# Kernel optimization log

Measured on AMD Instinct MI355X. Metric: run time of the kernel, lower is better.

The kernel has to match this reference:

```python
import jax, jax.numpy as jnp
import numpy as np

B, S, D = 8, 2048, 1024


def setup_inputs() -> dict:
    key = jax.random.key(0)
    ks = jax.random.split(key, 10)
    s = 0.02
    x = jax.random.normal(ks[0], (B, S, D), dtype=jnp.float32)
    # causal boolean mask [B, S, S]
    mask = jnp.broadcast_to(jnp.tril(jnp.ones((S, S), dtype=bool)), (B, S, S))
    Wq = jax.random.normal(ks[1], (D, D), dtype=jnp.float32) * s
    bq = jax.random.normal(ks[2], (D,), dtype=jnp.float32) * s
    Wk = jax.random.normal(ks[3], (D, D), dtype=jnp.float32) * s
    bk = jax.random.normal(ks[4], (D,), dtype=jnp.float32) * s
    Wv = jax.random.normal(ks[5], (D, D), dtype=jnp.float32) * s
    bv = jax.random.normal(ks[6], (D,), dtype=jnp.float32) * s
    Wo = jax.random.normal(ks[7], (D, D), dtype=jnp.float32) * s
    bo = jax.random.normal(ks[8], (D,), dtype=jnp.float32) * s
    return {"x": x, "mask": mask, "Wq": Wq, "bq": bq, "Wk": Wk, "bk": bk,
            "Wv": Wv, "bv": bv, "Wo": Wo, "bo": bo}


def reference(x, mask, Wq, bq, Wk, bk, Wv, bv, Wo, bo):
    # no cache -> cache_len = 0, full x/mask used; dropout=0.0 (identity)
    d_k = x.shape[-1]
    q = jnp.einsum('bsd,ed->bse', x, Wq) + bq
    k = jnp.einsum('bsd,ed->bse', x, Wk) + bk  # computed but unused (original bug)
    v = jnp.einsum('bsd,ed->bse', x, Wv) + bv
    # NOTE: original code uses q @ v^T (not k) - reproduced faithfully
    scores = jnp.einsum('bqd,bkd->bqk', q, v) / jnp.sqrt(jnp.float32(d_k))
    scores = jnp.where(mask, scores, jnp.float32(-jnp.inf))
    attn = jax.nn.softmax(scores, axis=-1)
    ctx = jnp.einsum('bqk,bkd->bqd', attn, v)
    out = jnp.einsum('bsd,ed->bse', ctx, Wo) + bo
    return out
```

## Files before the change

### kernel.cpp

```cpp
#include <hip/hip_runtime.h>

typedef unsigned short u16;
typedef __attribute__((ext_vector_type(8))) unsigned short u16x8;
typedef __bf16 bf16x8 __attribute__((ext_vector_type(8)));
typedef float f32x4 __attribute__((ext_vector_type(4)));

__device__ __forceinline__ u16 f2b(float f) {
    unsigned u = __float_as_uint(f);
    u += 0x7fffu + ((u >> 16) & 1u);
    return (u16)(u >> 16);
}
__device__ __forceinline__ float b2f(u16 h) {
    return __uint_as_float(((unsigned)h) << 16);
}

__device__ __forceinline__ void async_copy16(const void* g, void* l) {
    __builtin_amdgcn_global_load_lds(
        (const __attribute__((address_space(1))) unsigned int*)g,
        (__attribute__((address_space(3))) unsigned int*)l,
        16, 0, 0);
}

__device__ __forceinline__ int swz(int x) { return x ^ (((x >> 9) & 1) << 5); }

__global__ __launch_bounds__(256) void cast_kernel(const float* __restrict__ in,
                                                   u16* __restrict__ out, long n) {
    long i0 = ((long)blockIdx.x * 256 + threadIdx.x) * 8;
    long stride = (long)gridDim.x * 256 * 8;
    for (long i = i0; i < n; i += stride) {
        float4 a = *(const float4*)(in + i);
        float4 b = *(const float4*)(in + i + 4);
        u16x8 o;
        o[0] = f2b(a.x); o[1] = f2b(a.y); o[2] = f2b(a.z); o[3] = f2b(a.w);
        o[4] = f2b(b.x); o[5] = f2b(b.y); o[6] = f2b(b.z); o[7] = f2b(b.w);
        *(u16x8*)(out + i) = o;
    }
}

__global__ __launch_bounds__(256) void transpose_kernel(const u16* __restrict__ in,
                                                        u16* __restrict__ out,
                                                        int rows, int cols) {
    __shared__ u16 tile[32][33];
    long base = (long)blockIdx.z * rows * cols;
    const u16* I = in + base;
    u16* O = out + base;
    int r0 = blockIdx.y * 32, c0 = blockIdx.x * 32;
    int tx = threadIdx.x, ty = threadIdx.y;
    #pragma unroll
    for (int j = ty; j < 32; j += 8)
        tile[j][tx] = I[(long)(r0 + j) * cols + c0 + tx];
    __syncthreads();
    #pragma unroll
    for (int j = ty; j < 32; j += 8)
        O[(long)(c0 + j) * rows + r0 + tx] = tile[tx][j];
}

__global__ __launch_bounds__(256) void softmax_kernel(u16* __restrict__ Sc) {
    const int SS = 2048;
    long row = blockIdx.x;
    int q = (int)(row & (SS - 1));
    int L = q + 1;
    int Klim = ((q >> 8) + 1) << 8;
    u16* p = Sc + row * SS;
    int tid = threadIdx.x;

    float m = -1e30f;
    for (int i = tid; i < L; i += 256) m = fmaxf(m, b2f(p[i]));
    #pragma unroll
    for (int o = 32; o > 0; o >>= 1) m = fmaxf(m, __shfl_xor(m, o));
    __shared__ float redm[4];
    if ((tid & 63) == 0) redm[tid >> 6] = m;
    __syncthreads();
    m = fmaxf(fmaxf(redm[0], redm[1]), fmaxf(redm[2], redm[3]));

    float s = 0.f;
    for (int i = tid; i < L; i += 256) s += __expf(b2f(p[i]) - m);
    #pragma unroll
    for (int o = 32; o > 0; o >>= 1) s += __shfl_xor(s, o);
    __shared__ float reds[4];
    if ((tid & 63) == 0) reds[tid >> 6] = s;
    __syncthreads();
    s = reds[0] + reds[1] + reds[2] + reds[3];
    float inv = 1.f / s;

    for (int i = tid; i < Klim; i += 256) {
        float v = (i < L) ? __expf(b2f(p[i]) - m) * inv : 0.f;
        p[i] = f2b(v);
    }
}

template<typename OUTT, bool BIAS, bool CSKIP, bool KLIM>
__global__ __launch_bounds__(512)
void gemm256(const u16* __restrict__ Aall, const u16* __restrict__ Ball,
             const float* __restrict__ bias, OUTT* __restrict__ Call,
             int M, int N, int K, float scale, long sA, long sB, long sC) {
    const int bz = blockIdx.z;
    const u16* A = Aall + (long)bz * sA;
    const u16* B = Ball + (long)bz * sB;
    OUTT* C = Call + (long)bz * sC;
    const int bm = blockIdx.y, bn = blockIdx.x;
    if (CSKIP && bn > bm) return;
    int Keff = K;
    if (KLIM) { int kl = (bm + 1) * 256; Keff = kl < K ? kl : K; }
    const int NT = Keff >> 6;

    extern __shared__ __align__(16) char lds[];

    const int tid = threadIdx.x;
    const int lane = tid & 63;
    const int w = tid >> 6;
    const int wm = w >> 2, wn = w & 3;
    const int fr = lane & 15, hi = lane >> 4;
    const int axor = ((fr >> 2) & 1) << 5;

    const long rowA0 = (long)bm * 256;
    const long rowB0 = (long)bn * 256;

    auto stage_half = [&](const u16* mat, long gr0, int k0, char* region) {
        #pragma unroll
        for (int rd = 0; rd < 2; ++rd) {
            int pb = rd * 8192 + w * 1024;
            int p = pb + lane * 16;
            int L = swz(p);
            const u16* src = mat + (gr0 + (L >> 7)) * (long)K + k0 + ((L & 127) >> 1);
            async_copy16(src, region + pb);
        }
    };

    f32x4 acc[8][4] = {};
    bf16x8 a[4][2], b0[2][2], b1[2][2];

    char* bufp0 = lds;
    char* bufp1 = lds + 65536;

    stage_half(A, rowA0,       0, bufp0 + 0 * 16384);
    stage_half(B, rowB0,       0, bufp0 + 2 * 16384);
    stage_half(B, rowB0 + 128, 0, bufp0 + 3 * 16384);
    stage_half(A, rowA0 + 128, 0, bufp0 + 1 * 16384);
    asm volatile("s_waitcnt vmcnt(4)" ::: "memory");
    if (1 < NT) {
        stage_half(A, rowA0,       64, bufp1 + 0 * 16384);
        stage_half(B, rowB0,       64, bufp1 + 2 * 16384);
        stage_half(B, rowB0 + 128, 64, bufp1 + 3 * 16384);
    }
    asm volatile("s_waitcnt vmcnt(6)" ::: "memory");
    __builtin_amdgcn_s_barrier();

    const int abase = (wm * 64 + fr) * 128 + hi * 16;
    const int bbase = (wn * 32 + fr) * 128 + hi * 16;

    for (int u = 0; u < NT; ++u) {
        char* bufp  = (u & 1) ? bufp1 : bufp0;
        char* obufp = (u & 1) ? bufp0 : bufp1;

        #pragma unroll
        for (int m = 0; m < 4; ++m)
            #pragma unroll
            for (int kk = 0; kk < 2; ++kk)
                a[m][kk] = *(const bf16x8*)(bufp + 0 * 16384 + ((abase + m * 2048 + kk * 64) ^ axor));
        #pragma unroll
        for (int nl = 0; nl < 2; ++nl)
            #pragma unroll
            for (int kk = 0; kk < 2; ++kk)
                b0[nl][kk] = *(const bf16x8*)(bufp + 2 * 16384 + ((bbase + nl * 2048 + kk * 64) ^ axor));
        if (u + 1 < NT)
            stage_half(A, rowA0 + 128, (u + 1) * 64, obufp + 1 * 16384);
        asm volatile("s_waitcnt lgkmcnt(8)" ::: "memory");
        __builtin_amdgcn_s_barrier();
        asm volatile("s_waitcnt lgkmcnt(0)" ::: "memory");
        __builtin_amdgcn_sched_barrier(0);
        __builtin_amdgcn_s_setprio(1);
        #pragma unroll
        for (int m = 0; m < 4; ++m)
            #pragma unroll
            for (int nl = 0; nl < 2; ++nl)
                #pragma unroll
                for (int kk = 0; kk < 2; ++kk)
                    acc[m][nl] = __builtin_amdgcn_mfma_f32_16x16x32_bf16(a[m][kk], b0[nl][kk], acc[m][nl], 0, 0, 0);
        __builtin_amdgcn_s_setprio(0);
        __builtin_amdgcn_s_barrier();

        #pragma unroll
        for (int nl = 0; nl < 2; ++nl)
            #pragma unroll
            for (int kk = 0; kk < 2; ++kk)
                b1[nl][kk] = *(const bf16x8*)(bufp + 3 * 16384 + ((bbase + nl * 2048 + kk * 64) ^ axor));
        if (u + 2 < NT)
            stage_half(A, rowA0, (u + 2) * 64, bufp + 0 * 16384);
        __builtin_amdgcn_s_barrier();
        asm volatile("s_waitcnt lgkmcnt(0)" ::: "memory");
        __builtin_amdgcn_sched_barrier(0);
        __builtin_amdgcn_s_setprio(1);
        #pragma unroll
        for (int m = 0; m < 4; ++m)
            #pragma unroll
            for (int nl = 0; nl < 2; ++nl)
                #pragma unroll
                for (int kk = 0; kk < 2; ++kk)
                    acc[m][2 + nl] = __builtin_amdgcn_mfma_f32_16x16x32_bf16(a[m][kk], b1[nl][kk], acc[m][2 + nl], 0, 0, 0);
        __builtin_amdgcn_s_setprio(0);
        __builtin_amdgcn_s_barrier();

        #pragma unroll
        for (int m = 0; m < 4; ++m)
            #pragma unroll
            for (int kk = 0; kk < 2; ++kk)
                a[m][kk] = *(const bf16x8*)(bufp + 1 * 16384 + ((abase + m * 2048 + kk * 64) ^ axor));
        if (u + 2 < NT)
            stage_half(B, rowB0, (u + 2) * 64, bufp + 2 * 16384);
        __builtin_amdgcn_s_barrier();
        asm volatile("s_waitcnt lgkmcnt(0)" ::: "memory");
        __builtin_amdgcn_sched_barrier(0);
        __builtin_amdgcn_s_setprio(1);
        #pragma unroll
        for (int m = 0; m < 4; ++m)
            #pragma unroll
            for (int nl = 0; nl < 2; ++nl)
                #pragma unroll
                for (int kk = 0; kk < 2; ++kk)
                    acc[4 + m][2 + nl] = __builtin_amdgcn_mfma_f32_16x16x32_bf16(a[m][kk], b1[nl][kk], acc[4 + m][2 + nl], 0, 0, 0);
        __builtin_amdgcn_s_setprio(0);
        __builtin_amdgcn_s_barrier();

        if (u + 2 < NT)
            stage_half(B, rowB0 + 128, (u + 2) * 64, bufp + 3 * 16384);
        __builtin_amdgcn_s_barrier();
        __builtin_amdgcn_s_setprio(1);
        #pragma unroll
        for (int m = 0; m < 4; ++m)
            #pragma unroll
            for (int nl = 0; nl < 2; ++nl)
                #pragma unroll
                for (int kk = 0; kk < 2; ++kk)
                    acc[4 + m][nl] = __builtin_amdgcn_mfma_f32_16x16x32_bf16(a[m][kk], b0[nl][kk], acc[4 + m][nl], 0, 0, 0);
        __builtin_amdgcn_s_setprio(0);
        if (u < NT - 2) { asm volatile("s_waitcnt vmcnt(6)" ::: "memory"); }
        else            { asm volatile("s_waitcnt vmcnt(0)" ::: "memory"); }
        __builtin_amdgcn_s_barrier();
    }

    #pragma unroll
    for (int m = 0; m < 8; ++m) {
        int rl = (m < 4) ? (wm * 64 + m * 16) : (128 + wm * 64 + (m - 4) * 16);
        long grow = rowA0 + rl + hi * 4;
        #pragma unroll
        for (int n = 0; n < 4; ++n) {
            int cl = (n < 2) ? (wn * 32 + n * 16) : (128 + wn * 32 + (n - 2) * 16);
            long gcol = rowB0 + cl + fr;
            float bvv = BIAS ? bias[gcol] : 0.f;
            #pragma unroll
            for (int j = 0; j < 4; ++j) {
                float v = acc[m][n][j] * scale + bvv;
                if constexpr (sizeof(OUTT) == 2) {
                    C[(grow + j) * N + gcol] = (OUTT)f2b(v);
                } else {
                    C[(grow + j) * N + gcol] = v;
                }
            }
        }
    }
}

extern "C" void kernel_launch(void* const* d_in, const int* in_sizes, int n_in,
                              void* d_out, int out_size, void* d_ws, size_t ws_size,
                              hipStream_t stream) {
    (void)in_sizes; (void)n_in; (void)out_size; (void)ws_size;
    const float* x  = (const float*)d_in[0];
    const float* Wq = (const float*)d_in[2];
    const float* bq = (const float*)d_in[3];
    const float* Wv = (const float*)d_in[6];
    const float* bv = (const float*)d_in[7];
    const float* Wo = (const float*)d_in[8];
    const float* bo = (const float*)d_in[9];
    float* out = (float*)d_out;

    const long B = 8, S = 2048, D = 1024;
    const long MS = B * S;

    char* p = (char*)d_ws;
    u16* xb  = (u16*)p; p += MS * D * 2;
    u16* Wqb = (u16*)p; p += D * D * 2;
    u16* Wvb = (u16*)p; p += D * D * 2;
    u16* Wob = (u16*)p; p += D * D * 2;
    u16* Qb  = (u16*)p; p += MS * D * 2;
    u16* Vb  = (u16*)p; p += MS * D * 2;
    u16* Sb  = (u16*)p; p += B * S * S * 2;
    u16* ctxb = xb;
    u16* Vtb  = Qb;

    const int SMEM = 131072;
    (void)hipFuncSetAttribute((const void*)gemm256<u16, true, false, false>,
                              hipFuncAttributeMaxDynamicSharedMemorySize, SMEM);
    (void)hipFuncSetAttribute((const void*)gemm256<u16, false, true, false>,
                              hipFuncAttributeMaxDynamicSharedMemorySize, SMEM);
    (void)hipFuncSetAttribute((const void*)gemm256<u16, false, false, true>,
                              hipFuncAttributeMaxDynamicSharedMemorySize, SMEM);
    (void)hipFuncSetAttribute((const void*)gemm256<float, true, false, false>,
                              hipFuncAttributeMaxDynamicSharedMemorySize, SMEM);

    cast_kernel<<<4096, 256, 0, stream>>>(x, xb, MS * D);
    cast_kernel<<<512, 256, 0, stream>>>(Wq, Wqb, D * D);
    cast_kernel<<<512, 256, 0, stream>>>(Wv, Wvb, D * D);
    cast_kernel<<<512, 256, 0, stream>>>(Wo, Wob, D * D);

    dim3 gproj(D / 256, MS / 256, 1);
    gemm256<u16, true, false, false><<<gproj, 512, SMEM, stream>>>(
        xb, Wqb, bq, Qb, (int)MS, (int)D, (int)D, 1.0f, 0, 0, 0);
    gemm256<u16, true, false, false><<<gproj, 512, SMEM, stream>>>(
        xb, Wvb, bv, Vb, (int)MS, (int)D, (int)D, 1.0f, 0, 0, 0);

    dim3 gsc(S / 256, S / 256, B);
    gemm256<u16, false, true, false><<<gsc, 512, SMEM, stream>>>(
        Qb, Vb, nullptr, Sb, (int)S, (int)S, (int)D, 0.03125f, S * D, S * D, S * S);

    softmax_kernel<<<MS, 256, 0, stream>>>(Sb);

    dim3 gtr(D / 32, S / 32, B);
    transpose_kernel<<<gtr, dim3(32, 8), 0, stream>>>(Vb, Vtb, (int)S, (int)D);

    dim3 gpv(D / 256, S / 256, B);
    gemm256<u16, false, false, true><<<gpv, 512, SMEM, stream>>>(
        Sb, Vtb, nullptr, ctxb, (int)S, (int)D, (int)S, 1.0f, S * S, D * S, S * D);

    gemm256<float, true, false, false><<<gproj, 512, SMEM, stream>>>(
        ctxb, Wob, bo, out, (int)MS, (int)D, (int)D, 1.0f, 0, 0, 0);
}
```

Measured before the change: 559.0 us.

## Vectorize softmax and transpose, widen LDS swizzle, batch Q/V projections

Changes the LDS XOR swizzle in the GEMM from a single-bit pattern to a 3-bit, 16-byte-granular pattern to reduce bank conflicts on fragment reads. Softmax now reads and writes each row as 8-element vectors held in registers, so the row is loaded once instead of three times. The V transpose uses 64x64 tiles with 16-byte global accesses and a swizzled tile. The Q and V projections are merged into one launch via blockIdx.z, with a second bias pointer. The merged launch assumes Vb and Wvb sit at fixed offsets from Qb and Wqb in the workspace.

```diff
diff --git a/kernel.cpp b/kernel.cpp
--- a/kernel.cpp
+++ b/kernel.cpp
@@ -21,7 +21,7 @@
         16, 0, 0);
 }
 
-__device__ __forceinline__ int swz(int x) { return x ^ (((x >> 9) & 1) << 5); }
+__device__ __forceinline__ int swz(int x) { return x ^ (((x >> 7) & 7) << 4); }
 
 __global__ __launch_bounds__(256) void cast_kernel(const float* __restrict__ in,
                                                    u16* __restrict__ out, long n) {
@@ -39,20 +39,39 @@
 
 __global__ __launch_bounds__(256) void transpose_kernel(const u16* __restrict__ in,
                                                         u16* __restrict__ out,
-                                                        int rows, int cols) {
-    __shared__ u16 tile[32][33];
-    long base = (long)blockIdx.z * rows * cols;
-    const u16* I = in + base;
-    u16* O = out + base;
-    int r0 = blockIdx.y * 32, c0 = blockIdx.x * 32;
-    int tx = threadIdx.x, ty = threadIdx.y;
-    #pragma unroll
-    for (int j = ty; j < 32; j += 8)
-        tile[j][tx] = I[(long)(r0 + j) * cols + c0 + tx];
+                                                        int S_, int D_) {
+    __shared__ u16 tile[64 * 64];
+    long base = (long)blockIdx.z * (long)S_ * D_;
+    int r0 = blockIdx.y * 64;
+    int c0 = blockIdx.x * 64;
+    int t = threadIdx.x;
+    {
+        int r = t >> 3, cb = (t & 7) * 16;
+        #pragma unroll
+        for (int h = 0; h < 2; ++h) {
+            int rr = r + h * 32;
+            u16x8 d8 = *(const u16x8*)(in + base + (long)(r0 + rr) * D_ + c0 + (cb >> 1));
+            int phys = rr * 128 + (cb ^ (((rr >> 3) & 7) << 4));
+            *(u16x8*)((char*)tile + phys) = d8;
+        }
+    }
     __syncthreads();
-    #pragma unroll
-    for (int j = ty; j < 32; j += 8)
-        O[(long)(c0 + j) * rows + r0 + tx] = tile[tx][j];
+    {
+        int od = t & 63;
+        int gb = (t >> 6) * 2;
+        #pragma unroll
+        for (int h = 0; h < 2; ++h) {
+            int g = gb + h;
+            u16x8 o8;
+            #pragma unroll
+            for (int j = 0; j < 8; ++j) {
+                int rr = g * 8 + j;
+                int phys = rr * 128 + ((od * 2) ^ (((rr >> 3) & 7) << 4));
+                o8[j] = *(const u16*)((char*)tile + phys);
+            }
+            *(u16x8*)(out + base + (long)(c0 + od) * S_ + r0 + g * 8) = o8;
+        }
+    }
 }
 
 __global__ __launch_bounds__(256) void softmax_kernel(u16* __restrict__ Sc) {
@@ -63,41 +82,59 @@
     int Klim = ((q >> 8) + 1) << 8;
     u16* p = Sc + row * SS;
     int tid = threadIdx.x;
-
-    float m = -1e30f;
-    for (int i = tid; i < L; i += 256) m = fmaxf(m, b2f(p[i]));
+    int i0 = tid * 8;
+
+    float v[8];
+    if (i0 < Klim) {
+        u16x8 raw = *(const u16x8*)(p + i0);
+        #pragma unroll
+        for (int j = 0; j < 8; ++j)
+            v[j] = (i0 + j < L) ? b2f(raw[j]) : -1e30f;
+    } else {
+        #pragma unroll
+        for (int j = 0; j < 8; ++j) v[j] = -1e30f;
+    }
+
+    float m = v[0];
+    #pragma unroll
+    for (int j = 1; j < 8; ++j) m = fmaxf(m, v[j]);
     #pragma unroll
     for (int o = 32; o > 0; o >>= 1) m = fmaxf(m, __shfl_xor(m, o));
-    __shared__ float redm[4];
-    if ((tid & 63) == 0) redm[tid >> 6] = m;
+    __shared__ float red[8];
+    if ((tid & 63) == 0) red[tid >> 6] = m;
     __syncthreads();
-    m = fmaxf(fmaxf(redm[0], redm[1]), fmaxf(redm[2], redm[3]));
-
+    m = fmaxf(fmaxf(red[0], red[1]), fmaxf(red[2], red[3]));
+
+    float e[8];
     float s = 0.f;
-    for (int i = tid; i < L; i += 256) s += __expf(b2f(p[i]) - m);
+    #pragma unroll
+    for (int j = 0; j < 8; ++j) { e[j] = __expf(v[j] - m); s += e[j]; }
     #pragma unroll
     for (int o = 32; o > 0; o >>= 1) s += __shfl_xor(s, o);
-    __shared__ float reds[4];
-    if ((tid & 63) == 0) reds[tid >> 6] = s;
+    if ((tid & 63) == 0) red[4 + (tid >> 6)] = s;
     __syncthreads();
-    s = reds[0] + reds[1] + reds[2] + reds[3];
+    s = red[4] + red[5] + red[6] + red[7];
     float inv = 1.f / s;
 
-    for (int i = tid; i < Klim; i += 256) {
-        float v = (i < L) ? __expf(b2f(p[i]) - m) * inv : 0.f;
-        p[i] = f2b(v);
+    if (i0 < Klim) {
+        u16x8 o8;
+        #pragma unroll
+        for (int j = 0; j < 8; ++j) o8[j] = f2b(e[j] * inv);
+        *(u16x8*)(p + i0) = o8;
     }
 }
 
 template<typename OUTT, bool BIAS, bool CSKIP, bool KLIM>
 __global__ __launch_bounds__(512)
 void gemm256(const u16* __restrict__ Aall, const u16* __restrict__ Ball,
-             const float* __restrict__ bias, OUTT* __restrict__ Call,
+             const float* __restrict__ bias, const float* __restrict__ bias2,
+             OUTT* __restrict__ Call,
              int M, int N, int K, float scale, long sA, long sB, long sC) {
     const int bz = blockIdx.z;
     const u16* A = Aall + (long)bz * sA;
     const u16* B = Ball + (long)bz * sB;
     OUTT* C = Call + (long)bz * sC;
+    const float* bp = (bz && bias2) ? bias2 : bias;
     const int bm = blockIdx.y, bn = blockIdx.x;
     if (CSKIP && bn > bm) return;
     int Keff = K;
@@ -111,7 +148,7 @@
     const int w = tid >> 6;
     const int wm = w >> 2, wn = w & 3;
     const int fr = lane & 15, hi = lane >> 4;
-    const int axor = ((fr >> 2) & 1) << 5;
+    const int axor = (fr & 7) << 4;
 
     const long rowA0 = (long)bm * 256;
     const long rowB0 = (long)bn * 256;
@@ -121,8 +158,8 @@
         for (int rd = 0; rd < 2; ++rd) {
             int pb = rd * 8192 + w * 1024;
             int p = pb + lane * 16;
-            int L = swz(p);
-            const u16* src = mat + (gr0 + (L >> 7)) * (long)K + k0 + ((L & 127) >> 1);
+            int Lb = swz(p);
+            const u16* src = mat + (gr0 + (Lb >> 7)) * (long)K + k0 + ((Lb & 127) >> 1);
             async_copy16(src, region + pb);
         }
     };
@@ -247,7 +284,7 @@
         for (int n = 0; n < 4; ++n) {
             int cl = (n < 2) ? (wn * 32 + n * 16) : (128 + wn * 32 + (n - 2) * 16);
             long gcol = rowB0 + cl + fr;
-            float bvv = BIAS ? bias[gcol] : 0.f;
+            float bvv = BIAS ? bp[gcol] : 0.f;
             #pragma unroll
             for (int j = 0; j < 4; ++j) {
                 float v = acc[m][n][j] * scale + bvv;
@@ -303,25 +340,24 @@
     cast_kernel<<<512, 256, 0, stream>>>(Wv, Wvb, D * D);
     cast_kernel<<<512, 256, 0, stream>>>(Wo, Wob, D * D);
 
-    dim3 gproj(D / 256, MS / 256, 1);
-    gemm256<u16, true, false, false><<<gproj, 512, SMEM, stream>>>(
-        xb, Wqb, bq, Qb, (int)MS, (int)D, (int)D, 1.0f, 0, 0, 0);
-    gemm256<u16, true, false, false><<<gproj, 512, SMEM, stream>>>(
-        xb, Wvb, bv, Vb, (int)MS, (int)D, (int)D, 1.0f, 0, 0, 0);
+    dim3 gqv(D / 256, MS / 256, 2);
+    gemm256<u16, true, false, false><<<gqv, 512, SMEM, stream>>>(
+        xb, Wqb, bq, bv, Qb, (int)MS, (int)D, (int)D, 1.0f, 0, D * D, MS * D);
 
     dim3 gsc(S / 256, S / 256, B);
     gemm256<u16, false, true, false><<<gsc, 512, SMEM, stream>>>(
-        Qb, Vb, nullptr, Sb, (int)S, (int)S, (int)D, 0.03125f, S * D, S * D, S * S);
+        Qb, Vb, nullptr, nullptr, Sb, (int)S, (int)S, (int)D, 0.03125f, S * D, S * D, S * S);
 
     softmax_kernel<<<MS, 256, 0, stream>>>(Sb);
 
-    dim3 gtr(D / 32, S / 32, B);
-    transpose_kernel<<<gtr, dim3(32, 8), 0, stream>>>(Vb, Vtb, (int)S, (int)D);
+    dim3 gtr(D / 64, S / 64, B);
+    transpose_kernel<<<gtr, 256, 0, stream>>>(Vb, Vtb, (int)S, (int)D);
 
     dim3 gpv(D / 256, S / 256, B);
     gemm256<u16, false, false, true><<<gpv, 512, SMEM, stream>>>(
-        Sb, Vtb, nullptr, ctxb, (int)S, (int)D, (int)S, 1.0f, S * S, D * S, S * D);
-
+        Sb, Vtb, nullptr, nullptr, ctxb, (int)S, (int)D, (int)S, 1.0f, S * S, D * S, S * D);
+
+    dim3 gproj(D / 256, MS / 256, 1);
     gemm256<float, true, false, false><<<gproj, 512, SMEM, stream>>>(
-        ctxb, Wob, bo, out, (int)MS, (int)D, (int)D, 1.0f, 0, 0, 0);
-}
+        ctxb, Wob, bo, nullptr, out, (int)MS, (int)D, (int)D, 1.0f, 0, 0, 0);
+}
```

Measured after the change: 505.7 us. -9.5%, faster.
